# Kernel tuning notes

Hardware: AMD Instinct MI355X
Metric: run time of the kernel (lower is better)

The kernel has to match this reference:

```python
import jax, jax.numpy as jnp
import numpy as np
import itertools

B = 4
NSEM = 12                       # detected semantic classes
H, W = 480, 640
FOV = 79.0
VR = 100                        # vision_range (cells)
RES = 5.0                       # xy map resolution (cm/cell)
ZRES = 5.0                      # z resolution (cm/cell)
DU_SCALE = 1
AGENT_HEIGHT_CM = 88.0          # args.AGENT_HEIGHT * 100
MAX_H = int(360 / ZRES)         # 72
MIN_H = int(-40 / ZRES)         # -8
NZ = MAX_H - MIN_H              # 80
MAP_PRED_T = 1.0
EXP_PRED_T = 1.0
CAT_PRED_T = 5.0
F_CAM = (W / 2.0) / np.tan(np.deg2rad(FOV / 2.0))
XC = (W - 1) / 2.0
ZC = (H - 1) / 2.0
SHIFT_X = VR * int(RES) // 2    # shift_loc x = 250 cm (theta shift is identity)


def setup_inputs() -> dict:
    key = jax.random.key(0)
    k1, k2 = jax.random.split(key)
    # obs channels: [0:3]=rgb (unused), [3]=depth in cm, [4:]=semantic masks
    depth = jax.random.uniform(k1, (B, 1, H, W), jnp.float32) * 450.0 + 50.0
    sem = (jax.random.uniform(k2, (B, NSEM, H, W)) > 0.9).astype(jnp.float32)
    rgb = jnp.zeros((B, 3, H, W), jnp.float32)
    obs = jnp.concatenate([rgb, depth, sem], axis=1)
    return {"obs": obs}


def _splat_feat_3d(feat, coords, dims):
    """Trilinear splat (du.splat_feat_nd). feat:(B,F,N), coords:(B,3,N) in [-1,1]."""
    Bn, Fc, N = feat.shape
    flat = dims[0] * dims[1] * dims[2]
    grid = jnp.zeros((Bn, Fc, flat), feat.dtype)
    pos = [coords[:, d] * (dims[d] / 2.0) + dims[d] / 2.0 for d in range(3)]
    bi = jnp.arange(Bn)[:, None, None]
    fi = jnp.arange(Fc)[None, :, None]
    for corner in itertools.product((0, 1), repeat=3):
        wts = jnp.ones_like(pos[0])
        idx = jnp.zeros_like(pos[0])
        for d in range(3):
            p = jnp.floor(pos[d]) + corner[d]
            safe = ((p > 0) & (p < dims[d])).astype(feat.dtype)
            wts = wts * (1.0 - jnp.abs(pos[d] - p)) * safe
            idx = idx * dims[d] + p * safe
        iidx = idx.astype(jnp.int32)[:, None, :]
        grid = grid.at[bi, fi, iidx].add(feat * wts[:, None, :])
    return jnp.round(grid).reshape(Bn, Fc, *dims)


def reference(obs):
    depth = obs[:, 3]                                   # (B,H,W) cm
    xs = jnp.arange(W, dtype=obs.dtype)
    zs = jnp.arange(H, dtype=obs.dtype)
    # depth -> point cloud (du.get_point_cloud_from_z_t)
    x_pc = (xs[None, None, :] - XC) * depth / F_CAM
    z_pc = (ZC - zs[None, :, None]) * depth / F_CAM
    # camera->agent (elevation 0, +agent height), then shift_loc pose (theta term identity)
    x_w = x_pc + SHIFT_X
    y_w = depth
    z_w = z_pc + AGENT_HEIGHT_CM
    # standardize to [-1,1] grid coords
    x_std = (x_w / RES - VR // 2.0) / VR * 2.0
    y_std = (y_w / RES - VR // 2.0) / VR * 2.0
    z_std = (z_w / ZRES - (MAX_H + MIN_H) // 2.0) / (MAX_H - MIN_H) * 2.0
    N = (H // DU_SCALE) * (W // DU_SCALE)
    coords = jnp.stack([x_std.reshape(B, N), y_std.reshape(B, N), z_std.reshape(B, N)], axis=1)
    ones = jnp.ones((B, 1, N), obs.dtype)
    sem_feat = obs[:, 4:].reshape(B, NSEM, N)           # du_scale==1 -> avgpool is identity
    feat = jnp.concatenate([ones, sem_feat], axis=1)    # (B, 1+NSEM, N)
    voxels = _splat_feat_3d(feat, coords, (VR, VR, NZ))
    voxels = jnp.swapaxes(voxels, 2, 3)                 # (B, F, vr, vr, NZ)
    min_z = int(25 / ZRES - MIN_H)                      # 13
    max_z = int((AGENT_HEIGHT_CM + 1) / ZRES - MIN_H)   # 25
    agent_h = voxels[..., min_z:max_z].sum(-1)          # height-band sum
    all_h = voxels.sum(-1)                              # full-height sum
    fp_map = jnp.clip(agent_h[:, 0:1] / MAP_PRED_T, 0.0, 1.0)
    fp_exp = jnp.clip(all_h[:, 0:1] / EXP_PRED_T, 0.0, 1.0)
    sem_map = jnp.clip(agent_h[:, 1:] / CAT_PRED_T, 0.0, 1.0)
    return fp_map, fp_exp, sem_map
```

## Files before the change

kernel.cpp:

```cpp
#include <hip/hip_runtime.h>
#include <math.h>

constexpr int kB    = 4;
constexpr int kNSEM = 12;
constexpr int kH    = 480;
constexpr int kW    = 640;
constexpr int kNPIX = kH * kW;
constexpr int kNCH  = 16;
constexpr int kVR   = 100;
constexpr int kNZ   = 80;
constexpr int kZLO  = 13;
constexpr int kZHI  = 25;
constexpr int kNCELL  = kVR * kVR * kNZ;
constexpr int kNCHUNK = kNCELL / 256;

constexpr size_t A_CNT    = 0;
constexpr size_t A_PART   = (size_t)kNCELL * 4;
constexpr size_t A_COL    = A_PART + 12544;
constexpr size_t A_STRIDE = A_COL + (size_t)14 * 10000 * 4;


__device__ __forceinline__ float nofuse_f(float x) {
    asm volatile("" : "+v"(x));
    return x;
}

__device__ __forceinline__ void geom_f(int xi, int zi, float d, float rcpF,
                                       float& p0, float& p1, float& p2) {
    float tx  = ((float)xi - 319.5f) * d;
    float tz  = (239.5f - (float)zi) * d;
    float x_w = fmaf(tx, rcpF, 250.0f);
    float z_w = fmaf(tz, rcpF, 88.0f);
    p0 = x_w * 0.2f;
    p1 = d   * 0.2f;
    p2 = fmaf(z_w, 0.2f, 8.0f);
}

__device__ __forceinline__ bool cellmask(const float* __restrict__ ob, int pix,
                                         float rcpF, unsigned& cell, unsigned& mask,
                                         float& d, float& p0, float& p1, float& p2,
                                         bool want_mask) {
    int zi = pix / kW, xi = pix - zi * kW;
    d = ob[3 * kNPIX + pix];
    geom_f(xi, zi, d, rcpF, p0, p1, p2);
    int fx = (int)floorf(p0), fy = (int)floorf(p1), fz = (int)floorf(p2);
    if (fx < 0 || fx >= kVR || fy < 0 || fy >= kVR || fz < 0 || fz >= kNZ)
        return false;
    cell = ((unsigned)(fx * kVR + fy)) * (unsigned)kNZ + (unsigned)fz;
    mask = 0;
    if (want_mask) {
#pragma unroll
        for (int c = 0; c < kNSEM; ++c)
            if (ob[(4 + c) * kNPIX + pix] != 0.0f) mask |= (1u << c);
    }
    return true;
}

__global__ __launch_bounds__(256) void build_kernel(
        const float* __restrict__ obs, char* __restrict__ ws,
        int b0, int nb, float rcpF) {
    int t = blockIdx.x * blockDim.x + threadIdx.x;
    if (t >= nb * kNPIX) return;
    int lb = t / kNPIX, pix = t - lb * kNPIX;
    const float* ob = obs + (size_t)(b0 + lb) * kNCH * kNPIX;
    unsigned cell, mask; float d, p0, p1, p2;
    if (cellmask(ob, pix, rcpF, cell, mask, d, p0, p1, p2, false))
        atomicAdd((unsigned*)(ws + (size_t)lb * A_STRIDE + A_CNT) + cell, 1u);
}

__global__ __launch_bounds__(256) void scan_block_kernel(char* __restrict__ ws) {
    int blk = blockIdx.x, t = threadIdx.x;
    int lb = blk / kNCHUNK, chunk = blk - lb * kNCHUNK;
    char* base = ws + (size_t)lb * A_STRIDE;
    unsigned* cnt  = (unsigned*)(base + A_CNT);
    unsigned* part = (unsigned*)(base + A_PART);
    int i = chunk * 256 + t;
    unsigned v = cnt[i];
    __shared__ unsigned s[256];
    s[t] = v; __syncthreads();
#pragma unroll
    for (int dd = 1; dd < 256; dd <<= 1) {
        unsigned x = (t >= dd) ? s[t - dd] : 0u;
        __syncthreads();
        s[t] += x;
        __syncthreads();
    }
    cnt[i] = s[t] - v;
    if (t == 255) part[chunk] = s[255];
}

__global__ __launch_bounds__(256) void scan_partials_kernel(char* __restrict__ ws) {
    int lb = blockIdx.x, t = threadIdx.x;
    unsigned* p = (unsigned*)(ws + (size_t)lb * A_STRIDE + A_PART);
    const int per = (kNCHUNK + 255) / 256;
    int lo = t * per, hi = lo + per; if (hi > kNCHUNK) hi = kNCHUNK;
    unsigned sum = 0;
    for (int i = lo; i < hi; ++i) sum += p[i];
    __shared__ unsigned s[256];
    s[t] = sum; __syncthreads();
    unsigned own = sum;
#pragma unroll
    for (int dd = 1; dd < 256; dd <<= 1) {
        unsigned x = (t >= dd) ? s[t - dd] : 0u;
        __syncthreads();
        s[t] += x;
        __syncthreads();
    }
    unsigned running = s[t] - own;
    for (int i = lo; i < hi; ++i) {
        unsigned tmp = p[i]; p[i] = running; running += tmp;
    }
}

__global__ __launch_bounds__(256) void scan_add_kernel(char* __restrict__ ws) {
    int blk = blockIdx.x, t = threadIdx.x;
    int lb = blk / kNCHUNK, chunk = blk - lb * kNCHUNK;
    char* base = ws + (size_t)lb * A_STRIDE;
    unsigned* cnt = (unsigned*)(base + A_CNT);
    const unsigned* part = (const unsigned*)(base + A_PART);
    cnt[chunk * 256 + t] += part[chunk];
}

template <int ESZ>
__global__ __launch_bounds__(256) void scatter_kernel(
        const float* __restrict__ obs, char* __restrict__ ws,
        int b0, int nb, size_t entOff, float rcpF) {
    int t = blockIdx.x * blockDim.x + threadIdx.x;
    if (t >= nb * kNPIX) return;
    int lb = t / kNPIX, pix = t - lb * kNPIX;
    const float* ob = obs + (size_t)(b0 + lb) * kNCH * kNPIX;
    unsigned cell, mask; float d, p0, p1, p2;
    if (!cellmask(ob, pix, rcpF, cell, mask, d, p0, p1, p2, true)) return;
    unsigned slot = atomicAdd(
        (unsigned*)(ws + (size_t)lb * A_STRIDE + A_CNT) + cell, 1u);
    unsigned key = ((unsigned)pix << 12) | mask;
    char* entBase = ws + entOff + (size_t)lb * ((size_t)kNPIX * ESZ);
    if constexpr (ESZ == 16) {
        uint4 e; e.x = key; e.y = __float_as_uint(p0);
        e.z = __float_as_uint(p1); e.w = __float_as_uint(p2);
        ((uint4*)entBase)[slot] = e;
    } else if constexpr (ESZ == 8) {
        uint2 e; e.x = key; e.y = __float_as_uint(d);
        ((uint2*)entBase)[slot] = e;
    } else {
        ((unsigned*)entBase)[slot] = key;
    }
}

template <int ESZ>
__global__ __launch_bounds__(256) void sort_kernel(
        char* __restrict__ ws, int nb, size_t entOff) {
    int t = blockIdx.x * blockDim.x + threadIdx.x;
    if (t >= nb * kNCELL) return;
    int lb = t / kNCELL, c = t - lb * kNCELL;
    const unsigned* cnt = (const unsigned*)(ws + (size_t)lb * A_STRIDE + A_CNT);
    int lo = (c == 0) ? 0 : (int)cnt[c - 1];
    int hi = (int)cnt[c];
    char* entBase = ws + entOff + (size_t)lb * ((size_t)kNPIX * ESZ);
    if constexpr (ESZ == 16) {
        uint4* ent = (uint4*)entBase;
        for (int i = lo + 1; i < hi; ++i) {
            uint4 v = ent[i]; int j = i - 1;
            while (j >= lo && ent[j].x > v.x) { ent[j + 1] = ent[j]; --j; }
            ent[j + 1] = v;
        }
    } else if constexpr (ESZ == 8) {
        uint2* ent = (uint2*)entBase;
        for (int i = lo + 1; i < hi; ++i) {
            uint2 v = ent[i]; int j = i - 1;
            while (j >= lo && ent[j].x > v.x) { ent[j + 1] = ent[j]; --j; }
            ent[j + 1] = v;
        }
    } else {
        unsigned* ent = (unsigned*)entBase;
        for (int i = lo + 1; i < hi; ++i) {
            unsigned v = ent[i]; int j = i - 1;
            while (j >= lo && ent[j] > v) { ent[j + 1] = ent[j]; --j; }
            ent[j + 1] = v;
        }
    }
}

template <int ESZ>
__global__ __launch_bounds__(256) void gather_kernel(
        const float* __restrict__ obs, char* __restrict__ ws,
        int b0, int nb, size_t entOff, float rcpF) {
    const int perb = 99 * 99 * 79;
    int t = blockIdx.x * blockDim.x + threadIdx.x;
    if (t >= nb * perb) return;
    int lb = t / perb, r = t - lb * perb;
    int x = r / (99 * 79) + 1;
    int rem = r - (x - 1) * (99 * 79);
    int y = rem / 79 + 1;
    int z = rem - (y - 1) * 79 + 1;

    char* base = ws + (size_t)lb * A_STRIDE;
    const unsigned* cnt = (const unsigned*)(base + A_CNT);
    const char* entBase = ws + entOff + (size_t)lb * ((size_t)kNPIX * ESZ);
    const float* ob = obs + (size_t)(b0 + lb) * kNCH * kNPIX;

    bool win = (z >= kZLO) && (z < kZHI);
    float xf = (float)x, yf = (float)y, zf = (float)z;

    float s0 = 0.0f;
    float ssem[kNSEM];
#pragma unroll
    for (int c = 0; c < kNSEM; ++c) ssem[c] = 0.0f;

#pragma unroll
    for (int cc = 0; cc < 8; ++cc) {
        int c0 = (cc >> 2) & 1, c1 = (cc >> 1) & 1, c2 = cc & 1;
        unsigned cell = ((unsigned)((x - c0) * kVR + (y - c1))) * (unsigned)kNZ
                      + (unsigned)(z - c2);
        unsigned lo = (cell == 0u) ? 0u : cnt[cell - 1];
        unsigned hi = cnt[cell];
        for (unsigned k = lo; k < hi; ++k) {
            unsigned key; float p0, p1, p2;
            if constexpr (ESZ == 16) {
                uint4 e = ((const uint4*)entBase)[k];
                key = e.x;
                p0 = __uint_as_float(e.y);
                p1 = __uint_as_float(e.z);
                p2 = __uint_as_float(e.w);
            } else if constexpr (ESZ == 8) {
                uint2 e = ((const uint2*)entBase)[k];
                key = e.x;
                float d = __uint_as_float(e.y);
                int pix = (int)(key >> 12);
                int zi = pix / kW, xi = pix - zi * kW;
                geom_f(xi, zi, d, rcpF, p0, p1, p2);
            } else {
                key = ((const unsigned*)entBase)[k];
                int pix = (int)(key >> 12);
                int zi = pix / kW, xi = pix - zi * kW;
                float d = ob[3 * kNPIX + pix];
                geom_f(xi, zi, d, rcpF, p0, p1, p2);
            }
            float w0 = 1.0f - fabsf(p0 - xf);
            float w1 = 1.0f - fabsf(p1 - yf);
            float w2 = 1.0f - fabsf(p2 - zf);
            float wt = nofuse_f((w0 * w1) * w2);
            s0 += wt;
            if (win) {
                unsigned m = key & 0xFFFu;
#pragma unroll
                for (int c = 0; c < kNSEM; ++c)
                    if (m & (1u << c)) ssem[c] += wt;
            }
        }
    }

    float* col = (float*)(base + A_COL);
    int ij = y * kVR + x;
    float v0 = rintf(s0);
    if (v0 != 0.0f) {
        atomicAdd(col + 1 * 10000 + ij, v0);
        if (win) atomicAdd(col + 0 * 10000 + ij, v0);
    }
    if (win) {
#pragma unroll
        for (int c = 0; c < kNSEM; ++c) {
            float vc = rintf(ssem[c]);
            if (vc != 0.0f) atomicAdd(col + (2 + c) * 10000 + ij, vc);
        }
    }
}

__global__ __launch_bounds__(256) void finalize_kernel(
        const char* __restrict__ ws, float* __restrict__ out, int b0, int nb) {
    int t = blockIdx.x * blockDim.x + threadIdx.x;
    if (t >= nb * 14 * 10000) return;
    int lb = t / 140000, r = t - lb * 140000;
    int m = r / 10000, ij = r - m * 10000;
    int b = b0 + lb;
    const float* col = (const float*)(ws + (size_t)lb * A_STRIDE + A_COL);
    float v = col[m * 10000 + ij];
    if (m == 0)      out[b * 10000 + ij]              = fminf(fmaxf(v, 0.0f), 1.0f);
    else if (m == 1) out[kB * 10000 + b * 10000 + ij] = fminf(fmaxf(v, 0.0f), 1.0f);
    else             out[2 * kB * 10000 + (b * kNSEM + (m - 2)) * 10000 + ij]
                        = fminf(fmaxf(v * 0.2f, 0.0f), 1.0f);
}

template <int ESZ>
static void run_exact(const float* obs, float* out, char* ws,
                      int b0, int nb, float rcpF, hipStream_t stream) {
    size_t entOff = (size_t)nb * A_STRIDE;
    hipMemsetAsync(ws, 0, entOff, stream);
    int n1 = nb * kNPIX;
    build_kernel<<<(n1 + 255) / 256, 256, 0, stream>>>(obs, ws, b0, nb, rcpF);
    scan_block_kernel<<<nb * kNCHUNK, 256, 0, stream>>>(ws);
    scan_partials_kernel<<<nb, 256, 0, stream>>>(ws);
    scan_add_kernel<<<nb * kNCHUNK, 256, 0, stream>>>(ws);
    scatter_kernel<ESZ><<<(n1 + 255) / 256, 256, 0, stream>>>(obs, ws, b0, nb, entOff, rcpF);
    int n2 = nb * kNCELL;
    sort_kernel<ESZ><<<(n2 + 255) / 256, 256, 0, stream>>>(ws, nb, entOff);
    int n3 = nb * 99 * 99 * 79;
    gather_kernel<ESZ><<<(n3 + 255) / 256, 256, 0, stream>>>(obs, ws, b0, nb, entOff, rcpF);
    int n4 = nb * 14 * 10000;
    finalize_kernel<<<(n4 + 255) / 256, 256, 0, stream>>>(ws, out, b0, nb);
}

extern "C" void kernel_launch(void* const* d_in, const int* in_sizes, int n_in,
                              void* d_out, int out_size, void* d_ws, size_t ws_size,
                              hipStream_t stream) {
    const float* obs = (const float*)d_in[0];
    float* out = (float*)d_out;
    char* ws = (char*)d_ws;

    double rad = (79.0 / 2.0) * (M_PI / 180.0);
    float f_cam = (float)(640.0 / 2.0 / tan(rad));
    float rcpF  = 1.0f / f_cam;

    auto need = [](int nb, int esz) {
        return (size_t)nb * A_STRIDE + (size_t)nb * (size_t)kNPIX * esz;
    };

    if (ws_size >= need(4, 16)) {
        run_exact<16>(obs, out, ws, 0, kB, rcpF, stream);
    } else if (ws_size >= need(4, 8)) {
        run_exact<8>(obs, out, ws, 0, kB, rcpF, stream);
    } else if (ws_size >= need(1, 16)) {
        for (int b = 0; b < kB; ++b) run_exact<16>(obs, out, ws, b, 1, rcpF, stream);
    } else if (ws_size >= need(1, 8)) {
        for (int b = 0; b < kB; ++b) run_exact<8>(obs, out, ws, b, 1, rcpF, stream);
    } else {
        for (int b = 0; b < kB; ++b) run_exact<4>(obs, out, ws, b, 1, rcpF, stream);
    }
}
```

Measured before the change: 413.6 us.

## Stage neighbor column entries in LDS for the 16-byte gather path

Adds a gather kernel in which each block handles a 1x3 tile of (x,y) columns across all z. It loads the sorted entries of the 8 neighboring columns into shared memory once, so each voxel reads them from LDS rather than re-fetching overlapping entries from global memory. If the entries exceed the LDS capacity, the kernel falls back to global reads. The cost is that only 237 of 256 threads do gather work, plus extra setup syncs and serial column-base computation.

Measured after the change: 414.4 us. Within noise of the previous version (+0.2%).

```diff
diff --git a/kernel.cpp b/kernel.cpp
--- a/kernel.cpp
+++ b/kernel.cpp
@@ -18,7 +18,6 @@
 constexpr size_t A_PART   = (size_t)kNCELL * 4;
 constexpr size_t A_COL    = A_PART + 12544;
 constexpr size_t A_STRIDE = A_COL + (size_t)14 * 10000 * 4;
-
 
 __device__ __forceinline__ float nofuse_f(float x) {
     asm volatile("" : "+v"(x));
@@ -181,6 +180,112 @@
     }
 }
 
+constexpr int kCAP = 2048;
+__global__ __launch_bounds__(256) void gather_lds_kernel(
+        char* __restrict__ ws, int nb, size_t entOff) {
+    __shared__ uint4    sEnt[kCAP];
+    __shared__ unsigned sEndsRel[8][80];
+    __shared__ unsigned sCellcol[8], sLo[8], sLen[8], sColBase[8];
+    __shared__ unsigned sTotal;
+
+    const int per = 99 * 33;
+    int bid = blockIdx.x;
+    int lb = bid / per, r = bid - lb * per;
+    int x0 = r / 33 + 1;
+    int yt = r - (r / 33) * 33;
+    int y0 = yt * 3 + 1;
+
+    char* base = ws + (size_t)lb * A_STRIDE;
+    const unsigned* cnt = (const unsigned*)(base + A_CNT);
+    const uint4* entG = (const uint4*)(ws + entOff + (size_t)lb * ((size_t)kNPIX * 16));
+
+    int t = threadIdx.x;
+    if (t < 8) {
+        int jx = t >> 2, jy = t & 3;
+        int cx = x0 - 1 + jx, cy = y0 - 1 + jy;
+        unsigned cc = ((unsigned)(cx * kVR + cy)) * (unsigned)kNZ;
+        unsigned lo = (cc == 0u) ? 0u : cnt[cc - 1];
+        unsigned hi = cnt[cc + (kNZ - 1)];
+        sCellcol[t] = cc; sLo[t] = lo; sLen[t] = hi - lo;
+    }
+    __syncthreads();
+    if (t == 0) {
+        unsigned b = 0;
+        for (int j = 0; j < 8; ++j) { sColBase[j] = b; b += sLen[j]; }
+        sTotal = b;
+    }
+    __syncthreads();
+    for (int i = t; i < 8 * kNZ; i += 256) {
+        int j = i / kNZ, cz = i - j * kNZ;
+        sEndsRel[j][cz] = cnt[sCellcol[j] + cz] - sLo[j];
+    }
+    unsigned total = sTotal;
+    bool useLds = (total <= (unsigned)kCAP);
+    if (useLds) {
+        for (unsigned i = t; i < total; i += 256) {
+            int j = 0;
+            while (j < 7 && i >= sColBase[j + 1]) ++j;
+            sEnt[i] = entG[sLo[j] + (i - sColBase[j])];
+        }
+    }
+    __syncthreads();
+
+    if (t >= 3 * 79) return;
+    int yy = t / 79, zz = t - yy * 79;
+    int x = x0, y = y0 + yy, z = zz + 1;
+
+    bool win = (z >= kZLO) && (z < kZHI);
+    float xf = (float)x, yf = (float)y, zf = (float)z;
+
+    float s0 = 0.0f;
+    float ssem[kNSEM];
+#pragma unroll
+    for (int c = 0; c < kNSEM; ++c) ssem[c] = 0.0f;
+
+#pragma unroll
+    for (int cc8 = 0; cc8 < 8; ++cc8) {
+        int c0 = (cc8 >> 2) & 1, c1 = (cc8 >> 1) & 1, c2 = cc8 & 1;
+        int j = (c0 ^ 1) * 4 + (yy + 1 - c1);
+        int cz = z - c2;
+        unsigned e0 = cz ? sEndsRel[j][cz - 1] : 0u;
+        unsigned e1 = sEndsRel[j][cz];
+        unsigned ldsB = sColBase[j], glB = sLo[j];
+        for (unsigned k = e0; k < e1; ++k) {
+            uint4 e = useLds ? sEnt[ldsB + k] : entG[glB + k];
+            unsigned key = e.x;
+            float p0 = __uint_as_float(e.y);
+            float p1 = __uint_as_float(e.z);
+            float p2 = __uint_as_float(e.w);
+            float w0 = 1.0f - fabsf(p0 - xf);
+            float w1 = 1.0f - fabsf(p1 - yf);
+            float w2 = 1.0f - fabsf(p2 - zf);
+            float wt = nofuse_f((w0 * w1) * w2);
+            s0 += wt;
+            if (win) {
+                unsigned m = key & 0xFFFu;
+#pragma unroll
+                for (int c = 0; c < kNSEM; ++c)
+                    if (m & (1u << c)) ssem[c] += wt;
+            }
+        }
+    }
+
+    float* col = (float*)(base + A_COL);
+    int ij = y * kVR + x;
+    float v0 = rintf(s0);
+    if (v0 != 0.0f) {
+        atomicAdd(col + 1 * 10000 + ij, v0);
+        if (win) atomicAdd(col + 0 * 10000 + ij, v0);
+    }
+    if (win) {
+#pragma unroll
+        for (int c = 0; c < kNSEM; ++c) {
+            float vc = rintf(ssem[c]);
+            if (vc != 0.0f) atomicAdd(col + (2 + c) * 10000 + ij, vc);
+        }
+    }
+}
+
 template <int ESZ>
 __global__ __launch_bounds__(256) void gather_kernel(
         const float* __restrict__ obs, char* __restrict__ ws,
@@ -216,13 +321,7 @@
         unsigned hi = cnt[cell];
         for (unsigned k = lo; k < hi; ++k) {
             unsigned key; float p0, p1, p2;
-            if constexpr (ESZ == 16) {
-                uint4 e = ((const uint4*)entBase)[k];
-                key = e.x;
-                p0 = __uint_as_float(e.y);
-                p1 = __uint_as_float(e.z);
-                p2 = __uint_as_float(e.w);
-            } else if constexpr (ESZ == 8) {
+            if constexpr (ESZ == 8) {
                 uint2 e = ((const uint2*)entBase)[k];
                 key = e.x;
                 float d = __uint_as_float(e.y);
@@ -294,8 +393,12 @@
     scatter_kernel<ESZ><<<(n1 + 255) / 256, 256, 0, stream>>>(obs, ws, b0, nb, entOff, rcpF);
     int n2 = nb * kNCELL;
     sort_kernel<ESZ><<<(n2 + 255) / 256, 256, 0, stream>>>(ws, nb, entOff);
-    int n3 = nb * 99 * 99 * 79;
-    gather_kernel<ESZ><<<(n3 + 255) / 256, 256, 0, stream>>>(obs, ws, b0, nb, entOff, rcpF);
+    if constexpr (ESZ == 16) {
+        gather_lds_kernel<<<nb * 99 * 33, 256, 0, stream>>>(ws, nb, entOff);
+    } else {
+        int n3 = nb * 99 * 99 * 79;
+        gather_kernel<ESZ><<<(n3 + 255) / 256, 256, 0, stream>>>(obs, ws, b0, nb, entOff, rcpF);
+    }
     int n4 = nb * 14 * 10000;
     finalize_kernel<<<(n4 + 255) / 256, 256, 0, stream>>>(ws, out, b0, nb);
 }
```
